# Optimization experiments

Hardware: AMD Instinct MI355X
Metric: run time of the kernel (lower is better)

## Reference

```python
import jax, jax.numpy as jnp
import numpy as np

B, N, FIN, H, F = 8, 1024, 256, 8, 64
NEG_SLOPE = 0.2


def setup_inputs() -> dict:
    key = jax.random.key(0)
    k = jax.random.split(key, 6)
    x = jax.random.normal(k[0], (B, N, FIN), dtype=jnp.float32)
    adj_mask = jax.random.randint(k[1], (B, N, N), 0, 2, dtype=jnp.int32)
    edge_prior = jax.random.normal(k[2], (B, N, N), dtype=jnp.float32)
    # params (xavier-style scales)
    W = jax.random.normal(k[3], (FIN, H * F), dtype=jnp.float32) * np.sqrt(2.0 / (FIN + H * F))
    a_left = jax.random.normal(k[4], (H, F), dtype=jnp.float32) * np.sqrt(2.0 / (1 + F))
    a_right = jax.random.normal(k[5], (H, F), dtype=jnp.float32) * np.sqrt(2.0 / (1 + F))
    edge_scale = jnp.float32(0.05)
    return {"x": x, "adj_mask": adj_mask, "edge_prior": edge_prior,
            "W": W, "a_left": a_left, "a_right": a_right, "edge_scale": edge_scale}


def reference(x, adj_mask, edge_prior, W, a_left, a_right, edge_scale):
    b, n, _ = x.shape
    h = (x @ W).reshape(b, n, H, F)                      # [B,N,H,F]
    e_left = jnp.einsum('bnhf,hf->bnh', h, a_left)       # [B,N,H]
    e_right = jnp.einsum('bnhf,hf->bnh', h, a_right)     # [B,N,H]
    e = jax.nn.leaky_relu(e_left[:, :, None, :] + e_right[:, None, :, :],
                          negative_slope=NEG_SLOPE)      # [B,N,N,H]
    e = e + edge_scale * edge_prior[..., None]
    e = jnp.where((adj_mask == 0)[..., None], -jnp.inf, e)
    alpha = jax.nn.softmax(e, axis=2)                    # softmax over neighbors j
    h_new = jnp.einsum('bijh,bjhf->bihf', alpha, h)      # [B,N,H,F]
    return h_new.reshape(b, n, H * F)                    # concat=True
```

## Files before the change

kernel.cpp:

```cpp
#include <hip/hip_runtime.h>
#include <hip/hip_bf16.h>

#define B_ 8
#define N_ 1024
#define FIN_ 256
#define H_ 8
#define F_ 64
#define HF_ 512
#define BN_ 8192
#define LOG2E 1.4426950408889634f

using bf16x8 = __attribute__((ext_vector_type(8))) short;
using f32x4  = __attribute__((ext_vector_type(4))) float;
using i32x4  = __attribute__((ext_vector_type(4))) int;

__device__ __forceinline__ short f2bf(float x) {
  __hip_bfloat16 b = __float2bfloat16(x);
  return *reinterpret_cast<short*>(&b);
}
__device__ __forceinline__ float bf2f(short s) {
  union { unsigned u; float f; } v;
  v.u = ((unsigned)(unsigned short)s) << 16;
  return v.f;
}
__device__ __forceinline__ bf16x8 cvtCE(f32x4 pa, f32x4 pb, i32x4 ma, i32x4 mb, float es) {
  bf16x8 o;
#pragma unroll
  for (int e = 0; e < 4; e++) {
    o[e]     = f2bf(ma[e] != 0 ? es * pa[e] : -1e30f);
    o[e + 4] = f2bf(mb[e] != 0 ? es * pb[e] : -1e30f);
  }
  return o;
}

__global__ __launch_bounds__(256) void k_prep(
    const float* __restrict__ x, const float* __restrict__ W,
    const float* __restrict__ prior, const int* __restrict__ mask,
    const float* __restrict__ esp,
    short* __restrict__ xb, short* __restrict__ Wt, short* __restrict__ cmat) {
  const int bid = blockIdx.x;
  const int t   = threadIdx.x;
  if (bid >= 256) {
    const int cid = bid - 256;
    if (cid < 1024) {
      const int idx = (cid * 256 + t) * 8;
      f32x4 a = *(const f32x4*)(x + idx);
      f32x4 b = *(const f32x4*)(x + idx + 4);
      bf16x8 o;
      o[0]=f2bf(a[0]); o[1]=f2bf(a[1]); o[2]=f2bf(a[2]); o[3]=f2bf(a[3]);
      o[4]=f2bf(b[0]); o[5]=f2bf(b[1]); o[6]=f2bf(b[2]); o[7]=f2bf(b[3]);
      *(bf16x8*)(xb + idx) = o;
    } else {
      const int idx = (cid - 1024) * 256 + t;
      const int f = idx >> 8, c = idx & 255;
      Wt[f * FIN_ + c] = f2bf(W[c * HF_ + f]);
    }
    return;
  }
  __shared__ short stile[32768];
  const int b  = bid & 7;
  const int it = bid >> 3;
  const float es = esp[0] * LOG2E;
  const int r  = t >> 3;
  const int jb = (t & 7) * 8;
  const int frag = r >> 4, rl = r & 15;
  const size_t rowbase = ((size_t)b * N_ + it * 32 + r) * (size_t)N_;
#pragma unroll
  for (int jt = 0; jt < 16; jt++) {
    const int j = jt * 64 + jb;
    f32x4 p0 = *(const f32x4*)(prior + rowbase + j);
    f32x4 p1 = *(const f32x4*)(prior + rowbase + j + 4);
    i32x4 m0 = *(const i32x4*)(mask + rowbase + j);
    i32x4 m1 = *(const i32x4*)(mask + rowbase + j + 4);
    const int s = j >> 5;
    const int l = ((j >> 3) & 3) * 16 + rl;
    const int lsw = l ^ (2 * (l >> 4)) ^ ((s & 1) << 3);
    *(bf16x8*)(&stile[s * 1024 + frag * 512 + lsw * 8]) = cvtCE(p0, p1, m0, m1, es);
  }
  __syncthreads();
  short* cmt = cmat + (size_t)(b * 32 + it) * 32768;
#pragma unroll
  for (int k = 0; k < 16; k++) {
    const int g   = k * 2048 + t * 8;
    const int s   = g >> 10;
    const int rem = g & 1023;
    const int fr  = rem >> 9;
    const int l   = (rem >> 3) & 63;
    const int lsw = l ^ (2 * (l >> 4)) ^ ((s & 1) << 3);
    bf16x8 v = *(const bf16x8*)(&stile[s * 1024 + fr * 512 + lsw * 8]);
    *(bf16x8*)(cmt + g) = v;
  }
}

__global__ __launch_bounds__(256) void k_h(
    const short* __restrict__ Wt, const short* __restrict__ xb,
    const float* __restrict__ aL, const float* __restrict__ aR,
    short* __restrict__ hAg, float* __restrict__ el_t, float* __restrict__ er_t) {
  const int nt = blockIdx.x;
  const int h  = blockIdx.y;
  const int w  = threadIdx.x >> 6;
  const int l  = threadIdx.x & 63;
  const int lr = l & 15, lk = l >> 4;
  const int n0 = nt * 64;
  const int fbase = h * 64 + w * 16;

  f32x4 acc[4] = {};
  const short* arow = Wt + (fbase + lr) * FIN_ + lk * 8;

#pragma unroll
  for (int k0 = 0; k0 < FIN_; k0 += 32) {
    bf16x8 a = *(const bf16x8*)(arow + k0);
#pragma unroll
    for (int nf = 0; nf < 4; nf++) {
      bf16x8 bb = *(const bf16x8*)(xb + (size_t)(n0 + nf * 16 + lr) * FIN_ + k0 + lk * 8);
      acc[nf] = __builtin_amdgcn_mfma_f32_16x16x32_bf16(a, bb, acc[nf], 0, 0, 0);
    }
  }

  __shared__ short sT[64][72];
  __shared__ float sEl[4][64], sEr[4][64];
  float al[4], ar[4];
#pragma unroll
  for (int r = 0; r < 4; r++) {
    const int fl = w * 16 + lk * 4 + r;
    al[r] = aL[h * F_ + fl];
    ar[r] = aR[h * F_ + fl];
  }
#pragma unroll
  for (int nf = 0; nf < 4; nf++) {
    const int nl = nf * 16 + lr;
#pragma unroll
    for (int r = 0; r < 4; r++)
      sT[w * 16 + lk * 4 + r][nl] = f2bf(acc[nf][r]);
    float pl = acc[nf][0]*al[0] + acc[nf][1]*al[1] + acc[nf][2]*al[2] + acc[nf][3]*al[3];
    float pr = acc[nf][0]*ar[0] + acc[nf][1]*ar[1] + acc[nf][2]*ar[2] + acc[nf][3]*ar[3];
    pl += __shfl_xor(pl, 16); pl += __shfl_xor(pl, 32);
    pr += __shfl_xor(pr, 16); pr += __shfl_xor(pr, 32);
    if (lk == 0) { sEl[w][nl] = pl; sEr[w][nl] = pr; }
  }
  __syncthreads();
  if (threadIdx.x < 64) {
    const int n = threadIdx.x;
    el_t[h * BN_ + n0 + n] = (sEl[0][n] + sEl[1][n] + sEl[2][n] + sEl[3][n]) * LOG2E;
    er_t[h * BN_ + n0 + n] = (sEr[0][n] + sEr[1][n] + sEr[2][n] + sEr[3][n]) * LOG2E;
  }
  const int b8h = (nt >> 4) * 8 + h;
  const int jb  = (nt & 15) * 2;
#pragma unroll
  for (int gi = 0; gi < 2; gi++) {
    const int g   = threadIdx.x * 2 + gi;
    const int jsl = g >> 8, ff = (g >> 6) & 3, gl = g & 63;
    const int glr = gl & 15, glk = gl >> 4;
    bf16x8 v = *(const bf16x8*)(&sT[ff * 16 + glr][jsl * 32 + glk * 8]);
    *(bf16x8*)(hAg + (((size_t)b8h * 32 + jb + jsl) * 4 + ff) * 512 + gl * 8) = v;
  }
}

#define PREFX(sn, Hd, E0d, E1d, Cd)                                   \
  {                                                                   \
    const short* hs_ = hW + (size_t)(sn) * 2048;                      \
    Hd[0] = *(const bf16x8*)(hs_);                                    \
    Hd[1] = *(const bf16x8*)(hs_ + 512);                              \
    Hd[2] = *(const bf16x8*)(hs_ + 1024);                             \
    Hd[3] = *(const bf16x8*)(hs_ + 1536);                             \
    E0d   = *(const f32x4*)(erp + (sn) * 32);                         \
    E1d   = *(const f32x4*)(erp + (sn) * 32 + 4);                     \
    Cd[0] = *(const bf16x8*)(cmW + (size_t)(sn) * 1024);              \
    Cd[1] = *(const bf16x8*)(cmW + (size_t)(sn) * 1024 + 512);        \
  }

#define COMP2(Hu, Cu, E0u, E1u)                                                \
  {                                                                            \
    bf16x8 pfA, pfB;                                                           \
    _Pragma("unroll")                                                          \
    for (int q = 0; q < 4; q++) {                                              \
      const float e0 = E0u[q], e1 = E1u[q];                                    \
      float sA  = el0 + e0, sA2 = el0 + e1;                                    \
      float sB  = el1 + e0, sB2 = el1 + e1;                                    \
      float vA  = fmaf(0.6f, sA,  bf2f(Cu[0][q]));                             \
      vA  = fmaf(0.4f, fabsf(sA),  vA);                                        \
      float vA2 = fmaf(0.6f, sA2, bf2f(Cu[0][q + 4]));                         \
      vA2 = fmaf(0.4f, fabsf(sA2), vA2);                                       \
      float vB  = fmaf(0.6f, sB,  bf2f(Cu[1][q]));                             \
      vB  = fmaf(0.4f, fabsf(sB),  vB);                                        \
      float vB2 = fmaf(0.6f, sB2, bf2f(Cu[1][q + 4]));                         \
      vB2 = fmaf(0.4f, fabsf(sB2), vB2);                                       \
      pfA[q]     = f2bf(__builtin_amdgcn_exp2f(vA));                           \
      pfA[q + 4] = f2bf(__builtin_amdgcn_exp2f(vA2));                          \
      pfB[q]     = f2bf(__builtin_amdgcn_exp2f(vB));                           \
      pfB[q + 4] = f2bf(__builtin_amdgcn_exp2f(vB2));                          \
    }                                                                          \
    __builtin_amdgcn_s_setprio(1);                                             \
    accSA   = __builtin_amdgcn_mfma_f32_16x16x32_bf16(ones, pfA, accSA, 0,0,0);\
    accSB   = __builtin_amdgcn_mfma_f32_16x16x32_bf16(ones, pfB, accSB, 0,0,0);\
    accA[0] = __builtin_amdgcn_mfma_f32_16x16x32_bf16(Hu[0], pfA, accA[0],0,0,0);\
    accB[0] = __builtin_amdgcn_mfma_f32_16x16x32_bf16(Hu[0], pfB, accB[0],0,0,0);\
    accA[1] = __builtin_amdgcn_mfma_f32_16x16x32_bf16(Hu[1], pfA, accA[1],0,0,0);\
    accB[1] = __builtin_amdgcn_mfma_f32_16x16x32_bf16(Hu[1], pfB, accB[1],0,0,0);\
    accA[2] = __builtin_amdgcn_mfma_f32_16x16x32_bf16(Hu[2], pfA, accA[2],0,0,0);\
    accB[2] = __builtin_amdgcn_mfma_f32_16x16x32_bf16(Hu[2], pfB, accB[2],0,0,0);\
    accA[3] = __builtin_amdgcn_mfma_f32_16x16x32_bf16(Hu[3], pfA, accA[3],0,0,0);\
    accB[3] = __builtin_amdgcn_mfma_f32_16x16x32_bf16(Hu[3], pfB, accB[3],0,0,0);\
    __builtin_amdgcn_s_setprio(0);                                             \
  }

__global__ __launch_bounds__(512, 2) void k_attn(
    const short* __restrict__ hAg, const float* __restrict__ el_t,
    const float* __restrict__ er_t, const short* __restrict__ cmat,
    float* __restrict__ out) {
  const int bid = blockIdx.x;
  const int b  = bid & 7;
  const int it = bid >> 3;
  const int t  = threadIdx.x;
  const int h  = t >> 6;
  const int l  = t & 63;
  const int lr = l & 15, lk = l >> 4;
  const int i0 = it * 32;
  const size_t bn = (size_t)b * N_;

  const float el0 = el_t[h * BN_ + bn + i0 + lr];
  const float el1 = el_t[h * BN_ + bn + i0 + 16 + lr];
  const float* erp = er_t + h * BN_ + bn + lk * 8;
  const short* hW  = hAg + (size_t)(b * 8 + h) * 65536 + l * 8;
  const short* cmW = cmat + (size_t)(b * 32 + it) * 32768 + l * 8;

  bf16x8 HA[4], HB[4], HC[4], HD[4];
  bf16x8 cA[2], cB[2], cC[2], cD[2];
  f32x4 eA0, eA1, eB0, eB1, eC0, eC1, eD0, eD1;
  f32x4 accA[4] = {}, accB[4] = {};
  f32x4 accSA = {}, accSB = {};
  bf16x8 ones;
#pragma unroll
  for (int e = 0; e < 8; e++) ones[e] = (short)0x3F80;

  PREFX(0, HA, eA0, eA1, cA);
  PREFX(1, HB, eB0, eB1, cB);
  PREFX(2, HC, eC0, eC1, cC);
  PREFX(3, HD, eD0, eD1, cD);

  for (int s = 0; s < 32; s += 4) {
    COMP2(HA, cA, eA0, eA1);  PREFX(s + 4, HA, eA0, eA1, cA);
    COMP2(HB, cB, eB0, eB1);  PREFX(s + 5, HB, eB0, eB1, cB);
    COMP2(HC, cC, eC0, eC1);  PREFX(s + 6, HC, eC0, eC1, cC);
    COMP2(HD, cD, eD0, eD1);  PREFX(s + 7, HD, eD0, eD1, cD);
  }

  const float invA = 1.0f / accSA[0];
  const float invB = 1.0f / accSB[0];
  const size_t rowA = bn + i0 + lr;
  const size_t rowB = rowA + 16;
#pragma unroll
  for (int ff = 0; ff < 4; ff++) {
    f32x4 va = accA[ff], vb = accB[ff];
    va[0]*=invA; va[1]*=invA; va[2]*=invA; va[3]*=invA;
    vb[0]*=invB; vb[1]*=invB; vb[2]*=invB; vb[3]*=invB;
    *(f32x4*)(out + rowA * HF_ + h * 64 + ff * 16 + lk * 4) = va;
    *(f32x4*)(out + rowB * HF_ + h * 64 + ff * 16 + lk * 4) = vb;
  }
}

extern "C" void kernel_launch(void* const* d_in, const int* in_sizes, int n_in,
                              void* d_out, int out_size, void* d_ws, size_t ws_size,
                              hipStream_t stream) {
  const float* x     = (const float*)d_in[0];
  const int*   adj   = (const int*)  d_in[1];
  const float* prior = (const float*)d_in[2];
  const float* W     = (const float*)d_in[3];
  const float* aL    = (const float*)d_in[4];
  const float* aR    = (const float*)d_in[5];
  const float* es    = (const float*)d_in[6];
  float* out = (float*)d_out;

  char* ws = (char*)d_ws;
  short* hAg  = (short*)ws;
  short* xb   = (short*)(ws + 8u  * 1024 * 1024);
  short* Wt   = (short*)(ws + 12u * 1024 * 1024);
  float* el_t = (float*)(ws + 12u * 1024 * 1024 + 262144);
  float* er_t = (float*)(ws + 12u * 1024 * 1024 + 524288);
  short* cmat = (short*)(ws + 13u * 1024 * 1024);

  hipLaunchKernelGGL(k_prep, dim3(1792), dim3(256), 0, stream,
                     x, W, prior, adj, es, xb, Wt, cmat);
  hipLaunchKernelGGL(k_h,   dim3(128, 8), dim3(256), 0, stream,
                     Wt, xb, aL, aR, hAg, el_t, er_t);
  hipLaunchKernelGGL(k_attn, dim3(256), dim3(512), 0, stream,
                     hAg, el_t, er_t, cmat, out);
}
```

Before: 64.51 us.

## Split attention neighbor loop across waves with LDS reduction and double the grid

The attention kernel now gives each block four heads, not eight, and splits the 32 neighbor steps between two wave groups. The group handling the second half writes its partial accumulators and softmax sums to shared memory, and the first group adds them before normalising and storing. The grid doubles to 512 blocks with fewer prefetch registers per wave and launch bounds raised to 4 blocks per SM, to improve occupancy and load balance on the 256 CUs. In exchange it adds LDS traffic, a block barrier, and shallower prefetch pipelining (two stages instead of four).

```diff
diff --git a/kernel.cpp b/kernel.cpp
--- a/kernel.cpp
+++ b/kernel.cpp
@@ -204,19 +204,24 @@
     __builtin_amdgcn_s_setprio(0);                                             \
   }
 
-__global__ __launch_bounds__(512, 2) void k_attn(
+__global__ __launch_bounds__(512, 4) void k_attn(
     const short* __restrict__ hAg, const float* __restrict__ el_t,
     const float* __restrict__ er_t, const short* __restrict__ cmat,
     float* __restrict__ out) {
   const int bid = blockIdx.x;
   const int b  = bid & 7;
-  const int it = bid >> 3;
+  const int hp = (bid >> 3) & 1;
+  const int it = bid >> 4;
   const int t  = threadIdx.x;
-  const int h  = t >> 6;
+  const int w  = t >> 6;
+  const int h  = hp * 4 + (w & 3);
+  const int jh = w >> 2;
   const int l  = t & 63;
   const int lr = l & 15, lk = l >> 4;
   const int i0 = it * 32;
   const size_t bn = (size_t)b * N_;
+
+  __shared__ float red[4][64][36];
 
   const float el0 = el_t[h * BN_ + bn + i0 + lr];
   const float el1 = el_t[h * BN_ + bn + i0 + 16 + lr];
@@ -224,38 +229,58 @@
   const short* hW  = hAg + (size_t)(b * 8 + h) * 65536 + l * 8;
   const short* cmW = cmat + (size_t)(b * 32 + it) * 32768 + l * 8;
 
-  bf16x8 HA[4], HB[4], HC[4], HD[4];
-  bf16x8 cA[2], cB[2], cC[2], cD[2];
-  f32x4 eA0, eA1, eB0, eB1, eC0, eC1, eD0, eD1;
+  bf16x8 HA[4], HB[4];
+  bf16x8 cA[2], cB[2];
+  f32x4 eA0, eA1, eB0, eB1;
   f32x4 accA[4] = {}, accB[4] = {};
   f32x4 accSA = {}, accSB = {};
   bf16x8 ones;
 #pragma unroll
   for (int e = 0; e < 8; e++) ones[e] = (short)0x3F80;
 
-  PREFX(0, HA, eA0, eA1, cA);
-  PREFX(1, HB, eB0, eB1, cB);
-  PREFX(2, HC, eC0, eC1, cC);
-  PREFX(3, HD, eD0, eD1, cD);
-
-  for (int s = 0; s < 32; s += 4) {
-    COMP2(HA, cA, eA0, eA1);  PREFX(s + 4, HA, eA0, eA1, cA);
-    COMP2(HB, cB, eB0, eB1);  PREFX(s + 5, HB, eB0, eB1, cB);
-    COMP2(HC, cC, eC0, eC1);  PREFX(s + 6, HC, eC0, eC1, cC);
-    COMP2(HD, cD, eD0, eD1);  PREFX(s + 7, HD, eD0, eD1, cD);
-  }
-
-  const float invA = 1.0f / accSA[0];
-  const float invB = 1.0f / accSB[0];
-  const size_t rowA = bn + i0 + lr;
-  const size_t rowB = rowA + 16;
-#pragma unroll
-  for (int ff = 0; ff < 4; ff++) {
-    f32x4 va = accA[ff], vb = accB[ff];
-    va[0]*=invA; va[1]*=invA; va[2]*=invA; va[3]*=invA;
-    vb[0]*=invB; vb[1]*=invB; vb[2]*=invB; vb[3]*=invB;
-    *(f32x4*)(out + rowA * HF_ + h * 64 + ff * 16 + lk * 4) = va;
-    *(f32x4*)(out + rowB * HF_ + h * 64 + ff * 16 + lk * 4) = vb;
+  const int s0 = jh * 16;
+  PREFX(s0, HA, eA0, eA1, cA);
+  PREFX(s0 + 1, HB, eB0, eB1, cB);
+
+  for (int s = s0; s < s0 + 16; s += 2) {
+    COMP2(HA, cA, eA0, eA1);  PREFX(s + 2, HA, eA0, eA1, cA);
+    COMP2(HB, cB, eB0, eB1);  PREFX(s + 3, HB, eB0, eB1, cB);
+  }
+
+  if (jh) {
+    float* rb = &red[w & 3][l][0];
+#pragma unroll
+    for (int ff = 0; ff < 4; ff++)
+#pragma unroll
+      for (int e = 0; e < 4; e++) {
+        rb[ff * 4 + e]      = accA[ff][e];
+        rb[16 + ff * 4 + e] = accB[ff][e];
+      }
+    rb[32] = accSA[0];
+    rb[33] = accSB[0];
+  }
+  __syncthreads();
+  if (!jh) {
+    const float* rb = &red[w & 3][l][0];
+#pragma unroll
+    for (int ff = 0; ff < 4; ff++)
+#pragma unroll
+      for (int e = 0; e < 4; e++) {
+        accA[ff][e] += rb[ff * 4 + e];
+        accB[ff][e] += rb[16 + ff * 4 + e];
+      }
+    const float invA = 1.0f / (accSA[0] + rb[32]);
+    const float invB = 1.0f / (accSB[0] + rb[33]);
+    const size_t rowA = bn + i0 + lr;
+    const size_t rowB = rowA + 16;
+#pragma unroll
+    for (int ff = 0; ff < 4; ff++) {
+      f32x4 va = accA[ff], vb = accB[ff];
+      va[0]*=invA; va[1]*=invA; va[2]*=invA; va[3]*=invA;
+      vb[0]*=invB; vb[1]*=invB; vb[2]*=invB; vb[3]*=invB;
+      *(f32x4*)(out + rowA * HF_ + h * 64 + ff * 16 + lk * 4) = va;
+      *(f32x4*)(out + rowB * HF_ + h * 64 + ff * 16 + lk * 4) = vb;
+    }
   }
 }
 
@@ -283,6 +308,6 @@
                      x, W, prior, adj, es, xb, Wt, cmat);
   hipLaunchKernelGGL(k_h,   dim3(128, 8), dim3(256), 0, stream,
                      Wt, xb, aL, aR, hAg, el_t, er_t);
-  hipLaunchKernelGGL(k_attn, dim3(256), dim3(512), 0, stream,
+  hipLaunchKernelGGL(k_attn, dim3(512), dim3(512), 0, stream,
                      hAg, el_t, er_t, cmat, out);
 }
```

Result: slower. 104.3 us (+61.7%).

## Share per-head H tiles across waves via double-buffered LDS staging

Applied to the files above, without the earlier changes.

Each block now handles a single (batch, head) pair, and its 8 waves each cover different 32-row query tiles. Before, each wave was a different head and reloaded its own H slice from global memory. The H slice for the head is loaded cooperatively into a double-buffered shared-memory tile in chunks and read back by all waves. Only the edge-coefficient and e_right values are still prefetched per wave from global memory. This cuts redundant global traffic for H but adds 64KB of LDS per block, barriers between chunks, and fewer register prefetch stages, which may hurt occupancy under the launch bound of 2 blocks per CU.

```diff
diff --git a/kernel.cpp b/kernel.cpp
--- a/kernel.cpp
+++ b/kernel.cpp
@@ -156,17 +156,21 @@
   }
 }
 
-#define PREFX(sn, Hd, E0d, E1d, Cd)                                   \
+#define PREF_CE(sn, E0d, E1d, Cd)                                     \
   {                                                                   \
-    const short* hs_ = hW + (size_t)(sn) * 2048;                      \
-    Hd[0] = *(const bf16x8*)(hs_);                                    \
-    Hd[1] = *(const bf16x8*)(hs_ + 512);                              \
-    Hd[2] = *(const bf16x8*)(hs_ + 1024);                             \
-    Hd[3] = *(const bf16x8*)(hs_ + 1536);                             \
     E0d   = *(const f32x4*)(erp + (sn) * 32);                         \
     E1d   = *(const f32x4*)(erp + (sn) * 32 + 4);                     \
     Cd[0] = *(const bf16x8*)(cmW + (size_t)(sn) * 1024);              \
     Cd[1] = *(const bf16x8*)(cmW + (size_t)(sn) * 1024 + 512);        \
+  }
+
+#define PREF_HD(hb, sl, Hd)                                           \
+  {                                                                   \
+    const short* p_ = (hb) + (sl) * 2048 + l * 8;                     \
+    Hd[0] = *(const bf16x8*)(p_);                                     \
+    Hd[1] = *(const bf16x8*)(p_ + 512);                               \
+    Hd[2] = *(const bf16x8*)(p_ + 1024);                              \
+    Hd[3] = *(const bf16x8*)(p_ + 1536);                              \
   }
 
 #define COMP2(Hu, Cu, E0u, E1u)                                                \
@@ -210,39 +214,70 @@
     float* __restrict__ out) {
   const int bid = blockIdx.x;
   const int b  = bid & 7;
-  const int it = bid >> 3;
+  const int h  = (bid >> 3) & 7;
+  const int it = bid >> 6;
   const int t  = threadIdx.x;
-  const int h  = t >> 6;
+  const int w  = t >> 6;
   const int l  = t & 63;
   const int lr = l & 15, lk = l >> 4;
-  const int i0 = it * 32;
+  const int i0 = it * 256 + w * 32;
+  const int tw = it * 8 + w;
   const size_t bn = (size_t)b * N_;
+
+  __shared__ short hbuf[2][16384];
 
   const float el0 = el_t[h * BN_ + bn + i0 + lr];
   const float el1 = el_t[h * BN_ + bn + i0 + 16 + lr];
   const float* erp = er_t + h * BN_ + bn + lk * 8;
-  const short* hW  = hAg + (size_t)(b * 8 + h) * 65536 + l * 8;
-  const short* cmW = cmat + (size_t)(b * 32 + it) * 32768 + l * 8;
-
-  bf16x8 HA[4], HB[4], HC[4], HD[4];
-  bf16x8 cA[2], cB[2], cC[2], cD[2];
-  f32x4 eA0, eA1, eB0, eB1, eC0, eC1, eD0, eD1;
+  const short* cmW = cmat + (size_t)(b * 32 + tw) * 32768 + l * 8;
+  const short* hG  = hAg + (size_t)(b * 8 + h) * 65536;
+
+  bf16x8 stg0, stg1, stg2, stg3;
+#define SLOADH(c)                                                     \
+  { const short* p_ = hG + (c) * 16384 + t * 8;                       \
+    stg0 = *(const bf16x8*)(p_);        stg1 = *(const bf16x8*)(p_ + 4096); \
+    stg2 = *(const bf16x8*)(p_ + 8192); stg3 = *(const bf16x8*)(p_ + 12288); }
+#define SWRITEH(bufp)                                                 \
+  { short* q_ = (bufp) + t * 8;                                       \
+    *(bf16x8*)(q_)        = stg0;  *(bf16x8*)(q_ + 4096)  = stg1;     \
+    *(bf16x8*)(q_ + 8192) = stg2;  *(bf16x8*)(q_ + 12288) = stg3; }
+
+  bf16x8 HA[4], HB[4], cA[2], cB[2];
+  f32x4 eA0, eA1, eB0, eB1;
   f32x4 accA[4] = {}, accB[4] = {};
   f32x4 accSA = {}, accSB = {};
   bf16x8 ones;
 #pragma unroll
   for (int e = 0; e < 8; e++) ones[e] = (short)0x3F80;
 
-  PREFX(0, HA, eA0, eA1, cA);
-  PREFX(1, HB, eB0, eB1, cB);
-  PREFX(2, HC, eC0, eC1, cC);
-  PREFX(3, HD, eD0, eD1, cD);
-
-  for (int s = 0; s < 32; s += 4) {
-    COMP2(HA, cA, eA0, eA1);  PREFX(s + 4, HA, eA0, eA1, cA);
-    COMP2(HB, cB, eB0, eB1);  PREFX(s + 5, HB, eB0, eB1, cB);
-    COMP2(HC, cC, eC0, eC1);  PREFX(s + 6, HC, eC0, eC1, cC);
-    COMP2(HD, cD, eD0, eD1);  PREFX(s + 7, HD, eD0, eD1, cD);
+  SLOADH(0);
+  SWRITEH(&hbuf[0][0]);
+  SLOADH(1);
+  PREF_CE(0, eA0, eA1, cA);
+  PREF_CE(1, eB0, eB1, cB);
+  __syncthreads();
+
+  for (int ch = 0; ch < 4; ++ch) {
+    const short* hb = &hbuf[ch & 1][0];
+    const int s0 = ch * 8;
+    PREF_HD(hb, 0, HA);
+    PREF_HD(hb, 1, HB);
+#pragma unroll
+    for (int sl = 0; sl < 8; sl += 2) {
+      const int pa = (sl + 2 > 7) ? 7 : sl + 2;
+      const int pb = (sl + 3 > 7) ? 7 : sl + 3;
+      COMP2(HA, cA, eA0, eA1);
+      PREF_CE(s0 + sl + 2, eA0, eA1, cA);
+      PREF_HD(hb, pa, HA);
+      COMP2(HB, cB, eB0, eB1);
+      PREF_CE(s0 + sl + 3, eB0, eB1, cB);
+      PREF_HD(hb, pb, HB);
+    }
+    if (ch < 3) {
+      SWRITEH(&hbuf[(ch + 1) & 1][0]);
+      SLOADH(ch + 2 < 4 ? ch + 2 : 3);
+      __syncthreads();
+    }
   }
 
   const float invA = 1.0f / accSA[0];
```

Result: no change. 64.95 us (+0.7%).
